# Kernel tuning notes

Hardware: AMD Instinct MI355X
Metric: run time of the kernel (lower is better)

Reference implementation:

```python
import jax, jax.numpy as jnp
import numpy as np

CONV_CH, FRAG_DIM, N_P, N_T, PROJ = 32, 8, 6, 12, 64
B, T, W = 64, 256, 20


def _p(key, shape, scale=0.05):
    return (jax.random.normal(key, shape, dtype=jnp.float32) * scale)


def setup_inputs() -> dict:
    key = jax.random.key(0)
    ks = jax.random.split(key, 24)
    inp = {
        'pressure': jax.random.normal(ks[0], (B, T, W, N_P), dtype=jnp.float32),
        'torque': jax.random.normal(ks[1], (B, T, W, N_T), dtype=jnp.float32),
        'fragility': jax.random.uniform(ks[2], (B, 1), dtype=jnp.float32),
        # pressure encoder conv weights (O, I, K)
        'pw1': _p(ks[3], (CONV_CH, N_P, 3)), 'pb1': _p(ks[4], (CONV_CH,)),
        'pw2': _p(ks[5], (CONV_CH, CONV_CH, 3)), 'pb2': _p(ks[6], (CONV_CH,)),
        # torque encoder
        'tw1': _p(ks[7], (CONV_CH, N_T, 3)), 'tb1': _p(ks[8], (CONV_CH,)),
        'tw2': _p(ks[9], (CONV_CH, CONV_CH, 3)), 'tb2': _p(ks[10], (CONV_CH,)),
        # fragility Linear(1, 8)
        'fw': _p(ks[11], (FRAG_DIM, 1)), 'fb': _p(ks[12], (FRAG_DIM,)),
        # project Linear(72, 64)
        'prw': _p(ks[13], (PROJ, 2 * CONV_CH + FRAG_DIM)), 'prb': _p(ks[14], (PROJ,)),
        # LSTM (torch gate order i,f,g,o)
        'Wih': _p(ks[15], (4 * PROJ, PROJ)), 'Whh': _p(ks[16], (4 * PROJ, PROJ)),
        'bih': _p(ks[17], (4 * PROJ,)), 'bhh': _p(ks[18], (4 * PROJ,)),
        # head Linear(64, 4)
        'hw': _p(ks[19], (4, PROJ)), 'hb': _p(ks[20], (4,)),
    }
    return inp


def _conv1d(x, w, b):
    # x: (N, C, L), w: (O, I, K) -> (N, O, L-K+1), valid padding
    y = jax.lax.conv_general_dilated(x, w, (1,), 'VALID',
                                     dimension_numbers=('NCH', 'OIH', 'NCH'))
    return y + b[None, :, None]


def _encoder(x, w1, b1, w2, b2):
    # x: (N, C, L); conv-relu-conv-relu-global avg pool -> (N, CONV_CH)
    h = jax.nn.relu(_conv1d(x, w1, b1))
    h = jax.nn.relu(_conv1d(h, w2, b2))
    return jnp.mean(h, axis=-1)


def _lstm(x, Wih, Whh, bih, bhh):
    # x: (B, T, H); torch LSTM, gates i,f,g,o
    Bq, Tq, H = x.shape
    bias = bih + bhh
    xg = jnp.einsum('bth,gh->btg', x, Wih) + bias  # precompute input gates

    def step(carry, gt):
        h, c = carry
        g = gt + h @ Whh.T
        i, f, gg, o = jnp.split(g, 4, axis=-1)
        c = jax.nn.sigmoid(f) * c + jax.nn.sigmoid(i) * jnp.tanh(gg)
        h = jax.nn.sigmoid(o) * jnp.tanh(c)
        return (h, c), h

    init = (jnp.zeros((Bq, H), x.dtype), jnp.zeros((Bq, H), x.dtype))
    (hT, cT), hs = jax.lax.scan(step, init, xg.transpose(1, 0, 2))
    return hs.transpose(1, 0, 2), hT, cT


def reference(pressure, torque, fragility,
              pw1, pb1, pw2, pb2, tw1, tb1, tw2, tb2,
              fw, fb, prw, prb, Wih, Whh, bih, bhh, hw, hb):
    Bq, Tq = pressure.shape[:2]
    # batch all T windows at once: (B*T, C, L)
    p = pressure.reshape(Bq * Tq, W, N_P).transpose(0, 2, 1)
    t = torque.reshape(Bq * Tq, W, N_T).transpose(0, 2, 1)
    pf = _encoder(p, pw1, pb1, pw2, pb2)                    # (B*T, 32)
    tf = _encoder(t, tw1, tb1, tw2, tb2)                    # (B*T, 32)
    ff = jax.nn.relu(fragility @ fw.T + fb)                 # (B, 8)
    ff = jnp.broadcast_to(ff[:, None, :], (Bq, Tq, FRAG_DIM)).reshape(Bq * Tq, FRAG_DIM)
    cat = jnp.concatenate([pf, tf, ff], axis=1)             # (B*T, 72)
    feat = jax.nn.relu(cat @ prw.T + prb).reshape(Bq, Tq, PROJ)
    lstm_out, hT, cT = _lstm(feat, Wih, Whh, bih, bhh)
    out = jax.nn.sigmoid(lstm_out @ hw.T + hb)              # (B, T, 4)
    return out, hT, cT
```

## Files before the change

kernel.cpp:

```cpp
#include <hip/hip_runtime.h>
#include <math.h>

#define B_   64
#define T_   256
#define W_   20
#define NP_  6
#define NT_  12
#define CC_  32
#define FD_  8
#define PR_  64

#define LOG2E  1.4426950408889634f

typedef float v2f __attribute__((ext_vector_type(2)));
typedef _Float16 half2_t __attribute__((ext_vector_type(2)));

#define PINU(x) asm volatile("" : "+v"(x))
#define WAVE_SYNC() asm volatile("s_waitcnt lgkmcnt(0)" ::: "memory")

#define H2(u) __builtin_bit_cast(half2_t, (u))
#define EXP2N(x) __builtin_amdgcn_exp2f(x)

__device__ __forceinline__ unsigned packh2(float a, float b) {
    union { _Float16 h[2]; unsigned u; } cv;
    cv.h[0] = (_Float16)a; cv.h[1] = (_Float16)b;
    return cv.u;
}

__device__ __forceinline__ float sigmoidf_(float x) {
    return __builtin_amdgcn_rcpf(1.0f + EXP2N(-LOG2E * x));
}

#define W1PT_N  (18 * 64)
#define W2G_N   (64 * 48)
#define PRWT_N  (18 * 64 * 4)
#define WIHT_N  (16 * 4 * 64 * 4)
#define BSUM_N  256
#define PREP_TOTAL (W1PT_N + W2G_N + PRWT_N + WIHT_N + BSUM_N)

__global__ void prep_kernel(
    const float* __restrict__ pw1, const float* __restrict__ tw1,
    const float* __restrict__ pw2, const float* __restrict__ tw2,
    const float* __restrict__ prw, const float* __restrict__ Wih,
    const float* __restrict__ bih, const float* __restrict__ bhh,
    unsigned* __restrict__ w1pT, unsigned* __restrict__ w2g,
    float* __restrict__ prwT4, float* __restrict__ wihT4,
    float* __restrict__ bsum)
{
    int id = blockIdx.x * 256 + threadIdx.x;
    if (id < W1PT_N) {
        int lane = id & 63, m3 = id >> 6;
        int s = lane >> 5, o = lane & 31;
        int m = m3 / 3, k = m3 - 3 * m;
        unsigned v;
        if (s == 0)
            v = (m < 3) ? packh2(pw1[o * 18 + (2 * m) * 3 + k],
                                 pw1[o * 18 + (2 * m + 1) * 3 + k]) : 0u;
        else
            v = packh2(tw1[o * 36 + (2 * m) * 3 + k],
                       tw1[o * 36 + (2 * m + 1) * 3 + k]);
        w1pT[id] = v;
        return;
    }
    id -= W1PT_N;
    if (id < W2G_N) {
        int r = id / 48, c = id - 48 * r;
        int s = r >> 5, o = r & 31;
        int m = c / 3, k = c - 3 * m;
        const float* src = s ? tw2 : pw2;
        w2g[id] = packh2(src[o * 96 + (2 * m) * 3 + k],
                         src[o * 96 + (2 * m + 1) * 3 + k]);
        return;
    }
    id -= W2G_N;
    if (id < PRWT_N) {
        int j = id & 3, t = id >> 2;
        int lane = t & 63, kq = t >> 6;
        prwT4[id] = prw[lane * 72 + kq * 4 + j];
        return;
    }
    id -= PRWT_N;
    if (id < WIHT_N) {
        int j = id & 3, t = id >> 2;
        int lane = t & 63, gg = t >> 6;
        int gi = gg & 3, kq = gg >> 2;
        wihT4[id] = Wih[(gi * 64 + lane) * 64 + kq * 4 + j];
        return;
    }
    id -= WIHT_N;
    if (id < BSUM_N) bsum[id] = bih[id] + bhh[id];
}

__global__ __launch_bounds__(256, 4) void encoder_kernel(
    const float* __restrict__ pressure, const float* __restrict__ torque,
    const float* __restrict__ frag,
    const float* __restrict__ pb1, const float* __restrict__ tb1,
    const float* __restrict__ pb2, const float* __restrict__ tb2,
    const float* __restrict__ fw,  const float* __restrict__ fb,
    const float* __restrict__ prb,
    const unsigned* __restrict__ w1pT, const unsigned* __restrict__ w2g,
    const float* __restrict__ prwT4, const float* __restrict__ wihT4,
    const float* __restrict__ bsum,
    float* __restrict__ xg)
{
    const int tid  = threadIdx.x;
    const int wv   = tid >> 6;
    const int lane = tid & 63;
    const int bt   = blockIdx.x * 4 + wv;
    const int b    = bt >> 8;
    const int  o   = lane & 31;
    const bool isp = lane < 32;
    const int  s   = isp ? 0 : 1;

    __shared__ unsigned w2p[64 * 49];
    __shared__ __align__(16) unsigned xwp[4][2][120];
    __shared__ __align__(16) unsigned h1p[4][2][320];
    __shared__ __align__(16) float catb4[4][72];
    __shared__ __align__(16) float featsh4[4][64];

    float* catb   = catb4[wv];
    float* featsh = featsh4[wv];

    for (int idx = tid; idx < 64 * 48; idx += 256) {
        int r = idx / 48, c = idx - r * 48;
        w2p[r * 49 + c] = w2g[idx];
    }

    {
        unsigned* xz = &xwp[wv][0][0];
        #pragma unroll
        for (int idx = lane; idx < 240; idx += 64) xz[idx] = 0;
    }
    const float* pin = pressure + (size_t)bt * (W_ * NP_);
    for (int idx = lane; idx < W_ * NP_; idx += 64) {
        int w = idx / NP_, i = idx - w * NP_;
        ((_Float16*)&xwp[wv][0][(i >> 1) * 20 + w])[i & 1] = (_Float16)pin[idx];
    }
    const float* tin = torque + (size_t)bt * (W_ * NT_);
    for (int idx = lane; idx < W_ * NT_; idx += 64) {
        int w = idx / NT_, i = idx - w * NT_;
        ((_Float16*)&xwp[wv][1][(i >> 1) * 20 + w])[i & 1] = (_Float16)tin[idx];
    }
    if (lane < FD_) catb[64 + lane] = fmaxf(frag[b] * fw[lane] + fb[lane], 0.0f);

    unsigned w1p[18];
    #pragma unroll
    for (int m3 = 0; m3 < 18; ++m3) w1p[m3] = w1pT[m3 * 64 + lane];

    const float bz1 = isp ? pb1[o] : tb1[o];
    const float bz2 = isp ? pb2[o] : tb2[o];
    WAVE_SYNC();

    {
        const unsigned* xr = &xwp[wv][s][0];
        float acc[18];
        #pragma unroll
        for (int l = 0; l < 18; ++l) acc[l] = bz1;
        #pragma unroll
        for (int m = 0; m < 6; ++m) {
            uint4 r4[5];
            const uint4* rp = (const uint4*)(xr + m * 20);
            #pragma unroll
            for (int q = 0; q < 5; ++q) r4[q] = rp[q];
            const unsigned* rw = (const unsigned*)r4;
            const half2_t wk0 = H2(w1p[m * 3]), wk1 = H2(w1p[m * 3 + 1]), wk2 = H2(w1p[m * 3 + 2]);
            #pragma unroll
            for (int l = 0; l < 18; ++l) {
                float a = acc[l];
                a = __builtin_amdgcn_fdot2(wk0, H2(rw[l]),     a, false);
                a = __builtin_amdgcn_fdot2(wk1, H2(rw[l + 1]), a, false);
                a = __builtin_amdgcn_fdot2(wk2, H2(rw[l + 2]), a, false);
                acc[l] = a;
            }
        }
        #pragma unroll
        for (int l = 0; l < 18; ++l)
            ((_Float16*)&h1p[wv][s][(o >> 1) * 20 + l])[o & 1] = (_Float16)fmaxf(acc[l], 0.0f);
    }
    __syncthreads();

    {
        const unsigned* hr   = &h1p[wv][s][0];
        const unsigned* wrow = w2p + lane * 49;
        float sacc[16];
        #pragma unroll
        for (int l = 0; l < 16; ++l) sacc[l] = bz2;
        #pragma unroll 4
        for (int m = 0; m < 16; ++m) {
            uint4 r4[5];
            const uint4* rp = (const uint4*)(hr + m * 20);
            #pragma unroll
            for (int q = 0; q < 5; ++q) r4[q] = rp[q];
            const unsigned* rw = (const unsigned*)r4;
            const half2_t wk0 = H2(wrow[m * 3]), wk1 = H2(wrow[m * 3 + 1]), wk2 = H2(wrow[m * 3 + 2]);
            #pragma unroll
            for (int l = 0; l < 16; ++l) {
                float a = sacc[l];
                a = __builtin_amdgcn_fdot2(wk0, H2(rw[l]),     a, false);
                a = __builtin_amdgcn_fdot2(wk1, H2(rw[l + 1]), a, false);
                a = __builtin_amdgcn_fdot2(wk2, H2(rw[l + 2]), a, false);
                sacc[l] = a;
            }
        }
        float m2 = 0.0f;
        #pragma unroll
        for (int l = 0; l < 16; ++l) m2 += fmaxf(sacc[l], 0.0f);
        catb[lane] = m2 * 0.0625f;
    }
    WAVE_SYNC();

    {
        float acc = prb[lane];
        const float4* w4 = (const float4*)prwT4;
        const float4* c4 = (const float4*)catb;
        #pragma unroll
        for (int q = 0; q < 18; ++q) {
            float4 w = w4[q * 64 + lane];
            float4 cv = c4[q];
            acc += w.x * cv.x + w.y * cv.y + w.z * cv.z + w.w * cv.w;
        }
        featsh[lane] = fmaxf(acc, 0.0f);
    }
    WAVE_SYNC();

    {
        float4 fr[16];
        const float4* f4 = (const float4*)featsh;
        #pragma unroll
        for (int q = 0; q < 16; ++q) fr[q] = f4[q];
        float* xgrow = xg + (size_t)bt * 256;
        const float4* w44 = (const float4*)wihT4;
        #pragma unroll
        for (int gi = 0; gi < 4; ++gi) {
            float acc = bsum[gi * 64 + lane];
            #pragma unroll
            for (int q = 0; q < 16; ++q) {
                float4 w = w44[(q * 4 + gi) * 64 + lane];
                acc += w.x * fr[q].x + w.y * fr[q].y + w.z * fr[q].z + w.w * fr[q].w;
            }
            xgrow[gi * 64 + lane] = acc;
        }
    }
}

__global__ __launch_bounds__(64, 1) void lstm_kernel(
    const float* __restrict__ xg,
    const float* __restrict__ Whh,
    float* __restrict__ hout,
    float* __restrict__ dout)
{
    const int b = blockIdx.x;
    const int j = threadIdx.x;

    __shared__ __align__(16) _Float16 hs[64];

    unsigned wi[32], wf[32], wg[32], wo[32];
    {
        const v2f* ri = (const v2f*)(Whh + (size_t)(j)       * 64);
        const v2f* rf = (const v2f*)(Whh + (size_t)(64  + j) * 64);
        const v2f* rg = (const v2f*)(Whh + (size_t)(128 + j) * 64);
        const v2f* ro = (const v2f*)(Whh + (size_t)(192 + j) * 64);
        #pragma unroll
        for (int q = 0; q < 32; ++q) {
            v2f w;
            w = ri[q]; wi[q] = packh2(w.x, w.y);
            w = rf[q]; wf[q] = packh2(w.x, w.y);
            w = rg[q]; wg[q] = packh2(w.x, w.y);
            w = ro[q]; wo[q] = packh2(w.x, w.y);
        }
        #pragma unroll
        for (int q = 0; q < 32; ++q) { PINU(wi[q]); PINU(wf[q]); PINU(wg[q]); PINU(wo[q]); }
    }

    const float* xp = xg + (size_t)b * T_ * 256 + j;
    float4* hq4 = (float4*)(hout + (size_t)b * T_ * 64);

    float c = 0.0f;
    float h = 0.0f;
    hs[j] = (_Float16)0.0f;
    WAVE_SYNC();

    float xc0 = xp[0],   xc1 = xp[64],  xc2 = xp[128], xc3 = xp[192];
    float xn0 = xp[256], xn1 = xp[320], xn2 = xp[384], xn3 = xp[448];

    for (int tq = 0; tq < T_ / 4; ++tq) {
        float4 hacc;
        #pragma unroll
        for (int k = 0; k < 4; ++k) {
            const int t = tq * 4 + k;
            const int tp = ((t + 2 < T_) ? (t + 2) : (T_ - 1)) * 256;
            float xf0 = xp[tp], xf1 = xp[tp + 64], xf2 = xp[tp + 128], xf3 = xp[tp + 192];

            uint4 hb[8];
            const uint4* hp = (const uint4*)hs;
            #pragma unroll
            for (int q = 0; q < 8; ++q) hb[q] = hp[q];
            const unsigned* hu = (const unsigned*)hb;

            float ai0 = xc0, af0 = xc1, ag0 = xc2, ao0 = xc3;
            float ai1 = 0.0f, af1 = 0.0f, ag1 = 0.0f, ao1 = 0.0f;
            #pragma unroll
            for (int q = 0; q < 32; q += 2) {
                half2_t h0 = H2(hu[q]), h1 = H2(hu[q + 1]);
                ai0 = __builtin_amdgcn_fdot2(H2(wi[q]),     h0, ai0, false);
                af0 = __builtin_amdgcn_fdot2(H2(wf[q]),     h0, af0, false);
                ag0 = __builtin_amdgcn_fdot2(H2(wg[q]),     h0, ag0, false);
                ao0 = __builtin_amdgcn_fdot2(H2(wo[q]),     h0, ao0, false);
                ai1 = __builtin_amdgcn_fdot2(H2(wi[q + 1]), h1, ai1, false);
                af1 = __builtin_amdgcn_fdot2(H2(wf[q + 1]), h1, af1, false);
                ag1 = __builtin_amdgcn_fdot2(H2(wg[q + 1]), h1, ag1, false);
                ao1 = __builtin_amdgcn_fdot2(H2(wo[q + 1]), h1, ao1, false);
            }
            const float ai = ai0 + ai1, af = af0 + af1;
            const float ag = ag0 + ag1, ao = ao0 + ao1;

            const float I = __builtin_amdgcn_rcpf(1.0f + EXP2N(-LOG2E * ai));
            const float F = __builtin_amdgcn_rcpf(1.0f + EXP2N(-LOG2E * af));
            const float O = __builtin_amdgcn_rcpf(1.0f + EXP2N(-LOG2E * ao));
            const float rgv = __builtin_amdgcn_rcpf(1.0f + EXP2N((2.0f * LOG2E) * ag));
            const float IG  = __builtin_fmaf(-(I + I), rgv, I);
            c = __builtin_fmaf(F, c, IG);
            const float rcv = __builtin_amdgcn_rcpf(1.0f + EXP2N((2.0f * LOG2E) * c));
            h = __builtin_fmaf(-(O + O), rcv, O);

            hs[j] = (_Float16)h;
            (&hacc.x)[k] = h;

            xc0 = xn0; xc1 = xn1; xc2 = xn2; xc3 = xn3;
            xn0 = xf0; xn1 = xf1; xn2 = xf2; xn3 = xf3;
        }
        hq4[tq * 64 + j] = hacc;
    }

    dout[B_ * T_ * 4 + b * 64 + j]           = h;
    dout[B_ * T_ * 4 + B_ * 64 + b * 64 + j] = c;
}

__global__ __launch_bounds__(256) void head_kernel(
    const float* __restrict__ hout, const float* __restrict__ hw,
    const float* __restrict__ hb, float* __restrict__ out)
{
    const int blk = blockIdx.x;
    const int tid = threadIdx.x;

    __shared__ __align__(16) float hsh[64 * 68];
    __shared__ __align__(16) float wsh[256];
    __shared__ float bsh[4];

    const float4* s4 = (const float4*)(hout + (size_t)blk * 64 * 64);
    for (int q = tid; q < 1024; q += 256) {
        int tqL = q >> 6;
        int j   = q & 63;
        float4 v = s4[q];
        #pragma unroll
        for (int k = 0; k < 4; ++k)
            hsh[(tqL * 4 + k) * 68 + j] = (&v.x)[k];
    }
    if (tid < 64) ((float4*)wsh)[tid] = ((const float4*)hw)[tid];
    if (tid < 4)  bsh[tid] = hb[tid];
    __syncthreads();

    const int r = tid >> 2, m = tid & 3;
    const float4* hv = (const float4*)(hsh + r * 68);
    const float4* wv = (const float4*)(wsh + m * 64);
    float acc = bsh[m];
    #pragma unroll
    for (int q = 0; q < 16; ++q) {
        float4 a = hv[q], w = wv[q];
        acc += a.x * w.x + a.y * w.y + a.z * w.z + a.w * w.w;
    }
    out[(size_t)blk * 256 + tid] = sigmoidf_(acc);
}

extern "C" void kernel_launch(void* const* d_in, const int* in_sizes, int n_in,
                              void* d_out, int out_size, void* d_ws, size_t ws_size,
                              hipStream_t stream) {
    const float* pressure = (const float*)d_in[0];
    const float* torque   = (const float*)d_in[1];
    const float* frag     = (const float*)d_in[2];
    const float* pw1 = (const float*)d_in[3];
    const float* pb1 = (const float*)d_in[4];
    const float* pw2 = (const float*)d_in[5];
    const float* pb2 = (const float*)d_in[6];
    const float* tw1 = (const float*)d_in[7];
    const float* tb1 = (const float*)d_in[8];
    const float* tw2 = (const float*)d_in[9];
    const float* tb2 = (const float*)d_in[10];
    const float* fw  = (const float*)d_in[11];
    const float* fb  = (const float*)d_in[12];
    const float* prw = (const float*)d_in[13];
    const float* prb = (const float*)d_in[14];
    const float* Wih = (const float*)d_in[15];
    const float* Whh = (const float*)d_in[16];
    const float* bih = (const float*)d_in[17];
    const float* bhh = (const float*)d_in[18];
    const float* hw  = (const float*)d_in[19];
    const float* hb  = (const float*)d_in[20];

    float* out = (float*)d_out;

    float* xg   = (float*)d_ws;
    float* hout = xg + (size_t)B_ * T_ * 256;

    unsigned* w1pT = (unsigned*)hout;
    unsigned* w2g  = w1pT + W1PT_N;
    float*   prwT4 = (float*)(w2g + W2G_N);
    float*   wihT4 = prwT4 + PRWT_N;
    float*   bsumP = wihT4 + WIHT_N;

    prep_kernel<<<(PREP_TOTAL + 255) / 256, 256, 0, stream>>>(
        pw1, tw1, pw2, tw2, prw, Wih, bih, bhh,
        w1pT, w2g, prwT4, wihT4, bsumP);

    encoder_kernel<<<B_ * T_ / 4, 256, 0, stream>>>(
        pressure, torque, frag,
        pb1, tb1, pb2, tb2, fw, fb, prb,
        w1pT, w2g, prwT4, wihT4, bsumP, xg);

    lstm_kernel<<<B_, 64, 0, stream>>>(xg, Whh, hout, out);

    head_kernel<<<B_ * T_ / 64, 256, 0, stream>>>(hout, hw, hb, out);
}
```

Before: 196.0 us.

## Split LSTM recurrent matvec across two waves with LDS partial-sum reduction

The per-batch LSTM block grows from one wave to two. Each wave holds half of the Whh columns in registers and computes partial gate dot products over half of the hidden vector. The partials are exchanged through a double-buffered shared-memory array with a block barrier every timestep. Both waves then redundantly compute the gate nonlinearities and keep their own fp16 copy of h. This halves the serial fdot2 chain on the recurrent critical path but adds a __syncthreads and an LDS round-trip to each of the 256 sequential steps.

```diff
diff --git a/kernel.cpp b/kernel.cpp
--- a/kernel.cpp
+++ b/kernel.cpp
@@ -243,33 +243,35 @@
     }
 }
 
-__global__ __launch_bounds__(64, 1) void lstm_kernel(
+__global__ __launch_bounds__(128, 1) void lstm_kernel(
     const float* __restrict__ xg,
     const float* __restrict__ Whh,
     float* __restrict__ hout,
     float* __restrict__ dout)
 {
     const int b = blockIdx.x;
-    const int j = threadIdx.x;
-
-    __shared__ __align__(16) _Float16 hs[64];
-
-    unsigned wi[32], wf[32], wg[32], wo[32];
-    {
-        const v2f* ri = (const v2f*)(Whh + (size_t)(j)       * 64);
-        const v2f* rf = (const v2f*)(Whh + (size_t)(64  + j) * 64);
-        const v2f* rg = (const v2f*)(Whh + (size_t)(128 + j) * 64);
-        const v2f* ro = (const v2f*)(Whh + (size_t)(192 + j) * 64);
-        #pragma unroll
-        for (int q = 0; q < 32; ++q) {
-            v2f w;
-            w = ri[q]; wi[q] = packh2(w.x, w.y);
-            w = rf[q]; wf[q] = packh2(w.x, w.y);
-            w = rg[q]; wg[q] = packh2(w.x, w.y);
-            w = ro[q]; wo[q] = packh2(w.x, w.y);
-        }
-        #pragma unroll
-        for (int q = 0; q < 32; ++q) { PINU(wi[q]); PINU(wf[q]); PINU(wg[q]); PINU(wo[q]); }
+    const int j = threadIdx.x & 63;
+    const int w = threadIdx.x >> 6;
+
+    __shared__ __align__(16) _Float16 hs[2][64];
+    __shared__ __align__(16) float part[2][2][64][4];
+
+    unsigned wi[16], wf[16], wg[16], wo[16];
+    {
+        const v2f* ri = (const v2f*)(Whh + (size_t)(j)       * 64) + w * 16;
+        const v2f* rf = (const v2f*)(Whh + (size_t)(64  + j) * 64) + w * 16;
+        const v2f* rg = (const v2f*)(Whh + (size_t)(128 + j) * 64) + w * 16;
+        const v2f* ro = (const v2f*)(Whh + (size_t)(192 + j) * 64) + w * 16;
+        #pragma unroll
+        for (int q = 0; q < 16; ++q) {
+            v2f t;
+            t = ri[q]; wi[q] = packh2(t.x, t.y);
+            t = rf[q]; wf[q] = packh2(t.x, t.y);
+            t = rg[q]; wg[q] = packh2(t.x, t.y);
+            t = ro[q]; wo[q] = packh2(t.x, t.y);
+        }
+        #pragma unroll
+        for (int q = 0; q < 16; ++q) { PINU(wi[q]); PINU(wf[q]); PINU(wg[q]); PINU(wo[q]); }
     }
 
     const float* xp = xg + (size_t)b * T_ * 256 + j;
@@ -277,30 +279,37 @@
 
     float c = 0.0f;
     float h = 0.0f;
-    hs[j] = (_Float16)0.0f;
-    WAVE_SYNC();
-
-    float xc0 = xp[0],   xc1 = xp[64],  xc2 = xp[128], xc3 = xp[192];
-    float xn0 = xp[256], xn1 = xp[320], xn2 = xp[384], xn3 = xp[448];
+    hs[w][j] = (_Float16)0.0f;
+
+    float xc0 = 0.0f, xc1 = 0.0f, xc2 = 0.0f, xc3 = 0.0f;
+    float xn0 = 0.0f, xn1 = 0.0f, xn2 = 0.0f, xn3 = 0.0f;
+    if (w == 0) {
+        xc0 = xp[0];   xc1 = xp[64];  xc2 = xp[128]; xc3 = xp[192];
+        xn0 = xp[256]; xn1 = xp[320]; xn2 = xp[384]; xn3 = xp[448];
+    }
+    __syncthreads();
 
     for (int tq = 0; tq < T_ / 4; ++tq) {
         float4 hacc;
         #pragma unroll
         for (int k = 0; k < 4; ++k) {
-            const int t = tq * 4 + k;
-            const int tp = ((t + 2 < T_) ? (t + 2) : (T_ - 1)) * 256;
-            float xf0 = xp[tp], xf1 = xp[tp + 64], xf2 = xp[tp + 128], xf3 = xp[tp + 192];
-
-            uint4 hb[8];
-            const uint4* hp = (const uint4*)hs;
-            #pragma unroll
-            for (int q = 0; q < 8; ++q) hb[q] = hp[q];
+            float xf0, xf1, xf2, xf3;
+            if (w == 0) {
+                const int t = tq * 4 + k;
+                const int tp = ((t + 2 < T_) ? (t + 2) : (T_ - 1)) * 256;
+                xf0 = xp[tp]; xf1 = xp[tp + 64]; xf2 = xp[tp + 128]; xf3 = xp[tp + 192];
+            }
+
+            uint4 hb[4];
+            const uint4* hp = (const uint4*)(&((const unsigned*)hs[w])[w * 16]);
+            #pragma unroll
+            for (int q = 0; q < 4; ++q) hb[q] = hp[q];
             const unsigned* hu = (const unsigned*)hb;
 
             float ai0 = xc0, af0 = xc1, ag0 = xc2, ao0 = xc3;
             float ai1 = 0.0f, af1 = 0.0f, ag1 = 0.0f, ao1 = 0.0f;
             #pragma unroll
-            for (int q = 0; q < 32; q += 2) {
+            for (int q = 0; q < 16; q += 2) {
                 half2_t h0 = H2(hu[q]), h1 = H2(hu[q + 1]);
                 ai0 = __builtin_amdgcn_fdot2(H2(wi[q]),     h0, ai0, false);
                 af0 = __builtin_amdgcn_fdot2(H2(wf[q]),     h0, af0, false);
@@ -311,8 +320,17 @@
                 ag1 = __builtin_amdgcn_fdot2(H2(wg[q + 1]), h1, ag1, false);
                 ao1 = __builtin_amdgcn_fdot2(H2(wo[q + 1]), h1, ao1, false);
             }
-            const float ai = ai0 + ai1, af = af0 + af1;
-            const float ag = ag0 + ag1, ao = ao0 + ao1;
+
+            {
+                float4 p;
+                p.x = ai0 + ai1; p.y = af0 + af1; p.z = ag0 + ag1; p.w = ao0 + ao1;
+                *(float4*)part[k & 1][w][j] = p;
+            }
+            __syncthreads();
+            float4 o4 = *(const float4*)part[k & 1][w ^ 1][j];
+            float4 mine = *(const float4*)part[k & 1][w][j];
+            const float ai = mine.x + o4.x, af = mine.y + o4.y;
+            const float ag = mine.z + o4.z, ao = mine.w + o4.w;
 
             const float I = __builtin_amdgcn_rcpf(1.0f + EXP2N(-LOG2E * ai));
             const float F = __builtin_amdgcn_rcpf(1.0f + EXP2N(-LOG2E * af));
@@ -323,17 +341,21 @@
             const float rcv = __builtin_amdgcn_rcpf(1.0f + EXP2N((2.0f * LOG2E) * c));
             h = __builtin_fmaf(-(O + O), rcv, O);
 
-            hs[j] = (_Float16)h;
+            hs[w][j] = (_Float16)h;
             (&hacc.x)[k] = h;
 
-            xc0 = xn0; xc1 = xn1; xc2 = xn2; xc3 = xn3;
-            xn0 = xf0; xn1 = xf1; xn2 = xf2; xn3 = xf3;
-        }
-        hq4[tq * 64 + j] = hacc;
-    }
-
-    dout[B_ * T_ * 4 + b * 64 + j]           = h;
-    dout[B_ * T_ * 4 + B_ * 64 + b * 64 + j] = c;
+            if (w == 0) {
+                xc0 = xn0; xc1 = xn1; xc2 = xn2; xc3 = xn3;
+                xn0 = xf0; xn1 = xf1; xn2 = xf2; xn3 = xf3;
+            }
+        }
+        if (w == 0) hq4[tq * 64 + j] = hacc;
+    }
+
+    if (w == 0) {
+        dout[B_ * T_ * 4 + b * 64 + j]           = h;
+        dout[B_ * T_ * 4 + B_ * 64 + b * 64 + j] = c;
+    }
 }
 
 __global__ __launch_bounds__(256) void head_kernel(
@@ -417,7 +439,7 @@
         pb1, tb1, pb2, tb2, fw, fb, prb,
         w1pT, w2g, prwT4, wihT4, bsumP, xg);
 
-    lstm_kernel<<<B_, 64, 0, stream>>>(xg, Whh, hout, out);
+    lstm_kernel<<<B_, 128, 0, stream>>>(xg, Whh, hout, out);
 
     head_kernel<<<B_ * T_ / 64, 256, 0, stream>>>(hout, hw, hb, out);
 }
```

Result: slower. 205.2 us (+4.7%).
